# Performance work log

Hardware: AMD Instinct MI355X
Metric: run time of the kernel (lower is better)

## Reference

```python
import jax, jax.numpy as jnp
import numpy as np

H, W = 4096, 4096

# Fixed tiny kernels expressed as shifted-slice sums (exactly equivalent to
# F.conv2d with stride=1, padding=0 for these 0/1 kernels).

def _diag(x):   # [[1,0],[0,1]] -> (H-1, W-1)
    return x[:-1, :-1] + x[1:, 1:]

def _anti(x):   # [[0,1],[1,0]]
    return x[:-1, 1:] + x[1:, :-1]

def _all2(x):   # 2x2 all-ones
    return x[:-1, :-1] + x[:-1, 1:] + x[1:, :-1] + x[1:, 1:]

def _cross(x):  # 3x3 plus-shape -> (H-2, W-2)
    return x[:-2, 1:-1] + x[2:, 1:-1] + x[1:-1, :-2] + x[1:-1, 2:]

def setup_inputs() -> dict:
    key = jax.random.key(0)
    board = jax.random.randint(key, (H, W), 0, 3, dtype=jnp.int32)
    return {"board_np": board}

def reference(board_np):
    black = (board_np == 1).astype(jnp.float32)
    white = (board_np == 2).astype(jnp.float32)
    empty = (board_np == 0).astype(jnp.float32)

    black_diag, black_anti = _diag(black), _anti(black)
    white_diag, white_anti = _diag(white), _anti(white)
    empty_diag, empty_anti = _diag(empty), _anti(empty)

    bamboo_black = ((black_diag == 2) & (empty_anti == 2)) | ((black_anti == 2) & (empty_diag == 2))
    bamboo_white = ((white_diag == 2) & (empty_anti == 2)) | ((white_anti == 2) & (empty_diag == 2))

    black_s2, white_s2, empty_s2 = _all2(black), _all2(white), _all2(empty)
    # tmp_de/ae/be/ce: single-cell picks of the 2x2 window
    empty_d = empty[1:, 1:]
    empty_a = empty[:-1, :-1]
    empty_b = empty[:-1, 1:]
    empty_c = empty[1:, :-1]
    any_empty_corner = (empty_d == 1) | (empty_a == 1) | (empty_b == 1) | (empty_c == 1)

    tiger_black = (black_s2 >= 2) & any_empty_corner
    tiger_white = (white_s2 >= 2) & any_empty_corner
    empty_triangle_black = (black_s2 == 3) & (empty_s2 == 1)
    empty_triangle_white = (white_s2 == 3) & (empty_s2 == 1)

    empty_center = empty[1:-1, 1:-1]  # k_center conv
    eye_black = (empty_center == 1) & (_cross(black) == 4)
    eye_white = (empty_center == 1) & (_cross(white) == 4)

    return (bamboo_black, bamboo_white, tiger_black, tiger_white,
            empty_triangle_black, empty_triangle_white, eye_black, eye_white)
```

## Files before the change

kernel.cpp:

```cpp
#include <hip/hip_runtime.h>
#include <cstdint>


#define BW 4096
#define W1 4095
#define W2 4094
#define N1 16769025
#define N2 16760836
#define M55 0x5555u

typedef int i4a __attribute__((vector_size(16), aligned(16)));

struct Planes { unsigned pm[6]; unsigned em[2]; };

__device__ __forceinline__ Planes compute_swar(unsigned m0, unsigned m1, unsigned m2)
{
    const unsigned B0 = m0 & M55,        W0 = (m0 >> 1) & M55;
    const unsigned B1 = m1 & M55,        Wl = (m1 >> 1) & M55;
    const unsigned B2 = m2 & M55,        W2m = (m2 >> 1) & M55;
    const unsigned E0 = (B0 | W0) ^ M55;
    const unsigned E1 = (B1 | Wl) ^ M55;

    const unsigned sB0 = B0 >> 2, sB1 = B1 >> 2;
    const unsigned sW0 = W0 >> 2, sW1 = Wl >> 2;
    const unsigned sE0 = E0 >> 2, sE1 = E1 >> 2;
    const unsigned sB2 = B2 >> 2, sW2 = W2m >> 2;

    const unsigned EaEd = E0 & sE1;
    const unsigned EbEc = sE0 & E1;
    const unsigned anyE = E0 | sE0 | E1 | sE1;

    Planes r;
    {
        const unsigned P = B0 & sB0, Q = B1 & sB1;
        const unsigned Dg = B0 & sB1, Ag = sB0 & B1;
        const unsigned X = B0 & B1,  Y = sB0 & sB1;
        const unsigned ge2 = P | Q | Dg | Ag | X | Y;
        const unsigned ge3 = (P & (B1 | sB1)) | (Q & (B0 | sB0));
        r.pm[0] = (Dg & EbEc) | (Ag & EaEd);
        r.pm[2] = ge2 & anyE;
        r.pm[4] = ge3 & anyE;
        r.em[0] = sE1 & sB0 & B1 & (B1 >> 4) & sB2;
    }
    {
        const unsigned P = W0 & sW0, Q = Wl & sW1;
        const unsigned Dg = W0 & sW1, Ag = sW0 & Wl;
        const unsigned X = W0 & Wl,  Y = sW0 & sW1;
        const unsigned ge2 = P | Q | Dg | Ag | X | Y;
        const unsigned ge3 = (P & (Wl | sW1)) | (Q & (W0 | sW0));
        r.pm[1] = (Dg & EbEc) | (Ag & EaEd);
        r.pm[3] = ge2 & anyE;
        r.pm[5] = ge3 & anyE;
        r.em[1] = sE1 & sW0 & Wl & (Wl >> 4) & sW2;
    }
    return r;
}

template<int PH>
__device__ __forceinline__ void store_row(
    int* __restrict__ out, const int i, const int u, const bool has2,
    const Planes& pl)
{
    const bool fullv = (u < 1023);
    const size_t orow = (size_t)i * W1 + (u << 2);

    #pragma unroll
    for (int p = 0; p < 6; ++p) {
        const int sp = (PH - p) & 3;
        int* dst = out + (size_t)p * N1 + orow;
        if (fullv) {
            i4a s;
            s[0] = (int)((pl.pm[p] >> (2 * (sp + 0))) & 1);
            s[1] = (int)((pl.pm[p] >> (2 * (sp + 1))) & 1);
            s[2] = (int)((pl.pm[p] >> (2 * (sp + 2))) & 1);
            s[3] = (int)((pl.pm[p] >> (2 * (sp + 3))) & 1);
            *(i4a*)(dst + sp) = s;
        } else {
            #pragma unroll
            for (int k = 0; k < 3 - sp; ++k)
                dst[sp + k] = (int)((pl.pm[p] >> (2 * (sp + k))) & 1);
        }
        if (u == 0) {
            #pragma unroll
            for (int k = 0; k < sp; ++k)
                dst[k] = (int)((pl.pm[p] >> (2 * k)) & 1);
        }
    }

    if (has2) {
        const int e = (PH & 1) ? 0 : 2;
        int* d0 = out + (size_t)6 * N1 + (size_t)i * W2 + (u << 2);
        int* d1 = d0 + N2;
        if (fullv) {
            i4a s0, s1;
            #pragma unroll
            for (int k = 0; k < 4; ++k) {
                s0[k] = (int)((pl.em[0] >> (2 * (e + k))) & 1);
                s1[k] = (int)((pl.em[1] >> (2 * (e + k))) & 1);
            }
            *(i4a*)(d0 + e) = s0;
            *(i4a*)(d1 + e) = s1;
        } else if (e == 0) {
            #pragma unroll
            for (int k = 0; k < 2; ++k) {
                d0[k] = (int)((pl.em[0] >> (2 * k)) & 1);
                d1[k] = (int)((pl.em[1] >> (2 * k)) & 1);
            }
        }
        if (u == 0) {
            #pragma unroll
            for (int k = 0; k < e; ++k) {
                d0[k] = (int)((pl.em[0] >> (2 * k)) & 1);
                d1[k] = (int)((pl.em[1] >> (2 * k)) & 1);
            }
        }
    }
}

__global__ __launch_bounds__(256)
void motif_kernel(const int* __restrict__ board, int* __restrict__ out) {
    const int u  = blockIdx.x * 256 + threadIdx.x;
    const int i0 = blockIdx.y << 2;
    const int base = u << 2;
    const bool fullv = (u < 1023);
    const bool last = (i0 == W1 - 3);

    const int* pr[6];
    #pragma unroll
    for (int j = 0; j < 6; ++j) {
        int r = i0 + j; if (r > W1) r = W1;
        pr[j] = board + (size_t)r * BW + base;
    }
    i4a v[6], x[6];
    #pragma unroll
    for (int j = 0; j < 6; ++j) v[j] = *(const i4a*)pr[j];
    #pragma unroll
    for (int j = 0; j < 6; ++j) x[j] = (i4a){0,0,0,0};
    if (fullv) {
        #pragma unroll
        for (int j = 0; j < 6; ++j) x[j] = *(const i4a*)(pr[j] + 4);
    }

    auto pack = [](const i4a& vv, const i4a& xx) -> unsigned {
        return (unsigned)(vv[0] | (vv[1] << 2) | (vv[2] << 4) | (vv[3] << 6)
                        | (xx[0] << 8) | (xx[1] << 10) | (xx[2] << 12) | (xx[3] << 14));
    };
    unsigned m[6];
    #pragma unroll
    for (int j = 0; j < 6; ++j) m[j] = pack(v[j], x[j]);

    {
        Planes P = compute_swar(m[0], m[1], m[2]);
        store_row<0>(out, i0, u, true, P);
    }
    {
        Planes P = compute_swar(m[1], m[2], m[3]);
        store_row<1>(out, i0 + 1, u, true, P);
    }
    {
        Planes P = compute_swar(m[2], m[3], m[4]);
        store_row<2>(out, i0 + 2, u, !last, P);
    }
    if (!last) {
        Planes P = compute_swar(m[3], m[4], m[5]);
        store_row<3>(out, i0 + 3, u, true, P);
    }
}

extern "C" void kernel_launch(void* const* d_in, const int* in_sizes, int n_in,
                              void* d_out, int out_size, void* d_ws, size_t ws_size,
                              hipStream_t stream) {
    const int* board = (const int*)d_in[0];
    int* out = (int*)d_out;

    dim3 block(256, 1, 1);
    dim3 grid(4, 1024, 1);
    motif_kernel<<<grid, block, 0, stream>>>(board, out);
}
```

Baseline: 593.7 us.

## Split into bit-packed pack kernel and linear streaming expand kernel

Replaces the single fused kernel with two passes when a workspace is available. The first computes all eight motif planes as packed bits into a workspace of about 16 MB. The second walks the flat output linearly, decoding plane, row and column per 4-element chunk, so every store is a contiguous, aligned 16-byte write instead of the misaligned per-row stores used before. The cost is an extra launch, integer divisions per chunk and the bit-buffer round trip. The old kernel is kept as a fallback when no workspace is given.

Result: faster. 578.7 us, median of 2 (-2.5%).

```diff
diff --git a/kernel.cpp b/kernel.cpp
--- a/kernel.cpp
+++ b/kernel.cpp
@@ -5,8 +5,11 @@
 #define BW 4096
 #define W1 4095
 #define W2 4094
-#define N1 16769025
-#define N2 16760836
+#define N1 16769025u
+#define N2 16760836u
+#define TOTAL 134135822u
+#define PS 524160u
+#define NEED_BYTES 16773120u
 #define M55 0x5555u
 
 typedef int i4a __attribute__((vector_size(16), aligned(16)));
@@ -15,16 +18,16 @@
 
 __device__ __forceinline__ Planes compute_swar(unsigned m0, unsigned m1, unsigned m2)
 {
-    const unsigned B0 = m0 & M55,        W0 = (m0 >> 1) & M55;
+    const unsigned B0 = m0 & M55,        Wt = (m0 >> 1) & M55;
     const unsigned B1 = m1 & M55,        Wl = (m1 >> 1) & M55;
-    const unsigned B2 = m2 & M55,        W2m = (m2 >> 1) & M55;
-    const unsigned E0 = (B0 | W0) ^ M55;
+    const unsigned B2 = m2 & M55,        Wb = (m2 >> 1) & M55;
+    const unsigned E0 = (B0 | Wt) ^ M55;
     const unsigned E1 = (B1 | Wl) ^ M55;
 
     const unsigned sB0 = B0 >> 2, sB1 = B1 >> 2;
-    const unsigned sW0 = W0 >> 2, sW1 = Wl >> 2;
+    const unsigned sW0 = Wt >> 2, sW1 = Wl >> 2;
     const unsigned sE0 = E0 >> 2, sE1 = E1 >> 2;
-    const unsigned sB2 = B2 >> 2, sW2 = W2m >> 2;
+    const unsigned sB2 = B2 >> 2, sW2 = Wb >> 2;
 
     const unsigned EaEd = E0 & sE1;
     const unsigned EbEc = sE0 & E1;
@@ -43,11 +46,11 @@
         r.em[0] = sE1 & sB0 & B1 & (B1 >> 4) & sB2;
     }
     {
-        const unsigned P = W0 & sW0, Q = Wl & sW1;
-        const unsigned Dg = W0 & sW1, Ag = sW0 & Wl;
-        const unsigned X = W0 & Wl,  Y = sW0 & sW1;
+        const unsigned P = Wt & sW0, Q = Wl & sW1;
+        const unsigned Dg = Wt & sW1, Ag = sW0 & Wl;
+        const unsigned X = Wt & Wl,  Y = sW0 & sW1;
         const unsigned ge2 = P | Q | Dg | Ag | X | Y;
-        const unsigned ge3 = (P & (Wl | sW1)) | (Q & (W0 | sW0));
+        const unsigned ge3 = (P & (Wl | sW1)) | (Q & (Wt | sW0));
         r.pm[1] = (Dg & EbEc) | (Ag & EaEd);
         r.pm[3] = ge2 & anyE;
         r.pm[5] = ge3 & anyE;
@@ -55,6 +58,140 @@
     }
     return r;
 }
+
+
+__device__ __forceinline__ unsigned nib4(unsigned x) {
+    unsigned t = x & 0x55u;
+    t = (t | (t >> 1)) & 0x33u;
+    t = (t | (t >> 2)) & 0x0Fu;
+    return t;
+}
+
+__global__ __launch_bounds__(256)
+void pack_kernel(const int* __restrict__ board, uint32_t* __restrict__ bits)
+{
+    __shared__ uint8_t nib[32][256];
+    const int tid = threadIdx.x;
+    const int u   = blockIdx.x * 256 + tid;
+    const int i0  = blockIdx.y << 2;
+    const int base = u << 2;
+    const bool fullv = (u < 1023);
+
+    const int* pr6[6];
+    #pragma unroll
+    for (int j = 0; j < 6; ++j) {
+        int r = i0 + j; if (r > W1) r = W1;
+        pr6[j] = board + (size_t)r * BW + base;
+    }
+    i4a v[6], x[6];
+    #pragma unroll
+    for (int j = 0; j < 6; ++j) v[j] = *(const i4a*)pr6[j];
+    #pragma unroll
+    for (int j = 0; j < 6; ++j) x[j] = (i4a){0,0,0,0};
+    if (fullv) {
+        #pragma unroll
+        for (int j = 0; j < 6; ++j) x[j] = *(const i4a*)(pr6[j] + 4);
+    }
+
+    auto pack = [](const i4a& vv, const i4a& xx) -> unsigned {
+        return (unsigned)(vv[0] | (vv[1] << 2) | (vv[2] << 4) | (vv[3] << 6)
+                        | (xx[0] << 8) | (xx[1] << 10) | (xx[2] << 12) | (xx[3] << 14));
+    };
+    unsigned m[6];
+    #pragma unroll
+    for (int j = 0; j < 6; ++j) m[j] = pack(v[j], x[j]);
+
+    #pragma unroll
+    for (int r = 0; r < 4; ++r) {
+        Planes P = compute_swar(m[r], m[r + 1], m[r + 2]);
+        #pragma unroll
+        for (int p = 0; p < 6; ++p) nib[r * 8 + p][tid] = (uint8_t)nib4(P.pm[p]);
+        nib[r * 8 + 6][tid] = (uint8_t)nib4(P.em[0]);
+        nib[r * 8 + 7][tid] = (uint8_t)nib4(P.em[1]);
+    }
+    __syncthreads();
+
+    #pragma unroll
+    for (int k = 0; k < 4; ++k) {
+        const int wg  = tid + 256 * k;
+        const int pr  = wg >> 5, w_in = wg & 31;
+        const int r   = pr >> 3, p = pr & 7;
+        const int row = i0 + r;
+        const bool valid = (p < 6) ? (row <= 4094) : (row <= 4093);
+        if (valid) {
+            uint64_t t = *(const uint64_t*)&nib[pr][w_in * 8];
+            t &= 0x0F0F0F0F0F0F0F0Full;
+            t = (t | (t >> 4))  & 0x00FF00FF00FF00FFull;
+            t = (t | (t >> 8))  & 0x0000FFFF0000FFFFull;
+            t = (t | (t >> 16));
+            bits[(size_t)p * PS + (size_t)row * 128u
+                 + (unsigned)(blockIdx.x * 32 + w_in)] = (uint32_t)t;
+        }
+    }
+}
+
+__device__ __forceinline__ void decode(uint32_t e, uint32_t& p, uint32_t& row,
+                                       uint32_t& col, uint32_t& width)
+{
+    if (e < 6u * N1) {
+        p = e / N1;
+        const uint32_t rem = e - p * N1;
+        row = rem / W1;
+        col = rem - row * W1;
+        width = W1;
+    } else {
+        const uint32_t q  = e - 6u * N1;
+        const uint32_t pp = q / N2;
+        const uint32_t rem = q - pp * N2;
+        p = 6u + pp;
+        row = rem / W2;
+        col = rem - row * W2;
+        width = W2;
+    }
+}
+
+__global__ __launch_bounds__(256)
+void expand_kernel(const uint32_t* __restrict__ bits, int* __restrict__ out)
+{
+    const uint32_t c = blockIdx.x * 256u + threadIdx.x;
+    const uint32_t o = c * 4u;
+    if (o >= TOTAL) return;
+
+    uint32_t p, row, col, width;
+    decode(o, p, row, col, width);
+
+    if (col + 3u < width && o + 4u <= TOTAL) {
+        const uint32_t* wrow = bits + p * PS + row * 128u;
+        const uint32_t lo = col >> 5, sh = col & 31u;
+        const uint32_t w0 = wrow[lo];
+        const uint32_t w1 = wrow[lo + 1];
+        const uint32_t bv = (uint32_t)(((uint64_t)w0 | ((uint64_t)w1 << 32)) >> sh);
+        i4a s;
+        s[0] = (int)(bv & 1u);
+        s[1] = (int)((bv >> 1) & 1u);
+        s[2] = (int)((bv >> 2) & 1u);
+        s[3] = (int)((bv >> 3) & 1u);
+        *(i4a*)(out + o) = s;
+    } else {
+        int vals[4];
+        #pragma unroll
+        for (int k = 0; k < 4; ++k) {
+            const uint32_t e = o + (uint32_t)k;
+            if (e < TOTAL) {
+                uint32_t pp, rr, cc, ww;
+                decode(e, pp, rr, cc, ww);
+                vals[k] = (int)((bits[pp * PS + rr * 128u + (cc >> 5)] >> (cc & 31u)) & 1u);
+            } else vals[k] = 0;
+        }
+        if (o + 4u <= TOTAL) {
+            i4a s; s[0] = vals[0]; s[1] = vals[1]; s[2] = vals[2]; s[3] = vals[3];
+            *(i4a*)(out + o) = s;
+        } else {
+            for (uint32_t k = 0; o + k < TOTAL; ++k) out[o + k] = vals[k];
+        }
+    }
+}
+
 
 template<int PH>
 __device__ __forceinline__ void store_row(
@@ -149,23 +286,17 @@
     #pragma unroll
     for (int j = 0; j < 6; ++j) m[j] = pack(v[j], x[j]);
 
-    {
-        Planes P = compute_swar(m[0], m[1], m[2]);
-        store_row<0>(out, i0, u, true, P);
-    }
-    {
-        Planes P = compute_swar(m[1], m[2], m[3]);
-        store_row<1>(out, i0 + 1, u, true, P);
-    }
-    {
-        Planes P = compute_swar(m[2], m[3], m[4]);
-        store_row<2>(out, i0 + 2, u, !last, P);
-    }
+    {   Planes P = compute_swar(m[0], m[1], m[2]);
+        store_row<0>(out, i0, u, true, P); }
+    {   Planes P = compute_swar(m[1], m[2], m[3]);
+        store_row<1>(out, i0 + 1, u, true, P); }
+    {   Planes P = compute_swar(m[2], m[3], m[4]);
+        store_row<2>(out, i0 + 2, u, !last, P); }
     if (!last) {
         Planes P = compute_swar(m[3], m[4], m[5]);
-        store_row<3>(out, i0 + 3, u, true, P);
-    }
-}
+        store_row<3>(out, i0 + 3, u, true, P); }
+}
+
 
 extern "C" void kernel_launch(void* const* d_in, const int* in_sizes, int n_in,
                               void* d_out, int out_size, void* d_ws, size_t ws_size,
@@ -173,7 +304,13 @@
     const int* board = (const int*)d_in[0];
     int* out = (int*)d_out;
 
-    dim3 block(256, 1, 1);
-    dim3 grid(4, 1024, 1);
-    motif_kernel<<<grid, block, 0, stream>>>(board, out);
-}
+    if (d_ws != nullptr && ws_size >= (size_t)NEED_BYTES) {
+        uint32_t* bits = (uint32_t*)d_ws;
+        pack_kernel<<<dim3(4, 1024, 1), dim3(256, 1, 1), 0, stream>>>(board, bits);
+        const uint32_t chunks = (TOTAL + 3u) / 4u;
+        const uint32_t eblocks = (chunks + 255u) / 256u;
+        expand_kernel<<<dim3(eblocks, 1, 1), dim3(256, 1, 1), 0, stream>>>(bits, out);
+    } else {
+        motif_kernel<<<dim3(4, 1024, 1), dim3(256, 1, 1), 0, stream>>>(board, out);
+    }
+}
```

## Switch to output-indexed kernel with one aligned 4-wide store per thread

Applied to the files above, without the earlier changes.

Replaces the row-tiled kernel, in which each thread loaded six board rows and wrote all eight planes with misaligned partial stores, with a flat kernel where each thread owns four consecutive output elements. Each thread decodes plane, row and column by integer division, then loads only the few board cells it needs and runs the SWAR logic for a single plane before doing one aligned 16-byte store. This removes the unaligned and scalar edge writes. In exchange every plane reloads the board, giving about eight times more input reads (mostly cache hits), plus per-thread divisions and a scalar fallback for chunks that straddle rows.

Result: slower. 661.4 us (+11.4%).

```diff
diff --git a/kernel.cpp b/kernel.cpp
--- a/kernel.cpp
+++ b/kernel.cpp
@@ -5,8 +5,9 @@
 #define BW 4096
 #define W1 4095
 #define W2 4094
-#define N1 16769025
-#define N2 16760836
+#define N1 16769025u
+#define N2 16760836u
+#define TOTAL 134135822u
 #define M55 0x5555u
 
 typedef int i4a __attribute__((vector_size(16), aligned(16)));
@@ -15,16 +16,16 @@
 
 __device__ __forceinline__ Planes compute_swar(unsigned m0, unsigned m1, unsigned m2)
 {
-    const unsigned B0 = m0 & M55,        W0 = (m0 >> 1) & M55;
+    const unsigned B0 = m0 & M55,        Wt = (m0 >> 1) & M55;
     const unsigned B1 = m1 & M55,        Wl = (m1 >> 1) & M55;
-    const unsigned B2 = m2 & M55,        W2m = (m2 >> 1) & M55;
-    const unsigned E0 = (B0 | W0) ^ M55;
+    const unsigned B2 = m2 & M55,        Wb = (m2 >> 1) & M55;
+    const unsigned E0 = (B0 | Wt) ^ M55;
     const unsigned E1 = (B1 | Wl) ^ M55;
 
     const unsigned sB0 = B0 >> 2, sB1 = B1 >> 2;
-    const unsigned sW0 = W0 >> 2, sW1 = Wl >> 2;
+    const unsigned sW0 = Wt >> 2, sW1 = Wl >> 2;
     const unsigned sE0 = E0 >> 2, sE1 = E1 >> 2;
-    const unsigned sB2 = B2 >> 2, sW2 = W2m >> 2;
+    const unsigned sB2 = B2 >> 2, sW2 = Wb >> 2;
 
     const unsigned EaEd = E0 & sE1;
     const unsigned EbEc = sE0 & E1;
@@ -43,11 +44,11 @@
         r.em[0] = sE1 & sB0 & B1 & (B1 >> 4) & sB2;
     }
     {
-        const unsigned P = W0 & sW0, Q = Wl & sW1;
-        const unsigned Dg = W0 & sW1, Ag = sW0 & Wl;
-        const unsigned X = W0 & Wl,  Y = sW0 & sW1;
+        const unsigned P = Wt & sW0, Q = Wl & sW1;
+        const unsigned Dg = Wt & sW1, Ag = sW0 & Wl;
+        const unsigned X = Wt & Wl,  Y = sW0 & sW1;
         const unsigned ge2 = P | Q | Dg | Ag | X | Y;
-        const unsigned ge3 = (P & (Wl | sW1)) | (Q & (W0 | sW0));
+        const unsigned ge3 = (P & (Wl | sW1)) | (Q & (Wt | sW0));
         r.pm[1] = (Dg & EbEc) | (Ag & EaEd);
         r.pm[3] = ge2 & anyE;
         r.pm[5] = ge3 & anyE;
@@ -56,114 +57,112 @@
     return r;
 }
 
-template<int PH>
-__device__ __forceinline__ void store_row(
-    int* __restrict__ out, const int i, const int u, const bool has2,
-    const Planes& pl)
+__device__ __forceinline__ void decode(uint32_t e, uint32_t& p, uint32_t& row,
+                                       uint32_t& col, uint32_t& width)
 {
-    const bool fullv = (u < 1023);
-    const size_t orow = (size_t)i * W1 + (u << 2);
-
-    #pragma unroll
-    for (int p = 0; p < 6; ++p) {
-        const int sp = (PH - p) & 3;
-        int* dst = out + (size_t)p * N1 + orow;
-        if (fullv) {
-            i4a s;
-            s[0] = (int)((pl.pm[p] >> (2 * (sp + 0))) & 1);
-            s[1] = (int)((pl.pm[p] >> (2 * (sp + 1))) & 1);
-            s[2] = (int)((pl.pm[p] >> (2 * (sp + 2))) & 1);
-            s[3] = (int)((pl.pm[p] >> (2 * (sp + 3))) & 1);
-            *(i4a*)(dst + sp) = s;
-        } else {
-            #pragma unroll
-            for (int k = 0; k < 3 - sp; ++k)
-                dst[sp + k] = (int)((pl.pm[p] >> (2 * (sp + k))) & 1);
-        }
-        if (u == 0) {
-            #pragma unroll
-            for (int k = 0; k < sp; ++k)
-                dst[k] = (int)((pl.pm[p] >> (2 * k)) & 1);
-        }
-    }
-
-    if (has2) {
-        const int e = (PH & 1) ? 0 : 2;
-        int* d0 = out + (size_t)6 * N1 + (size_t)i * W2 + (u << 2);
-        int* d1 = d0 + N2;
-        if (fullv) {
-            i4a s0, s1;
-            #pragma unroll
-            for (int k = 0; k < 4; ++k) {
-                s0[k] = (int)((pl.em[0] >> (2 * (e + k))) & 1);
-                s1[k] = (int)((pl.em[1] >> (2 * (e + k))) & 1);
-            }
-            *(i4a*)(d0 + e) = s0;
-            *(i4a*)(d1 + e) = s1;
-        } else if (e == 0) {
-            #pragma unroll
-            for (int k = 0; k < 2; ++k) {
-                d0[k] = (int)((pl.em[0] >> (2 * k)) & 1);
-                d1[k] = (int)((pl.em[1] >> (2 * k)) & 1);
-            }
-        }
-        if (u == 0) {
-            #pragma unroll
-            for (int k = 0; k < e; ++k) {
-                d0[k] = (int)((pl.em[0] >> (2 * k)) & 1);
-                d1[k] = (int)((pl.em[1] >> (2 * k)) & 1);
-            }
-        }
+    if (e < 6u * N1) {
+        p = e / N1;
+        const uint32_t rem = e - p * N1;
+        row = rem / W1;
+        col = rem - row * W1;
+        width = W1;
+    } else {
+        const uint32_t q  = e - 6u * N1;
+        const uint32_t pp = q / N2;
+        const uint32_t rem = q - pp * N2;
+        p = 6u + pp;
+        row = rem / W2;
+        col = rem - row * W2;
+        width = W2;
     }
 }
 
+__device__ __forceinline__ int one_out(const int* __restrict__ board,
+                                       uint32_t p, uint32_t row, uint32_t col)
+{
+    if (p < 6u) {
+        const int a = board[(size_t)row * BW + col];
+        const int b = board[(size_t)row * BW + col + 1];
+        const int c = board[(size_t)(row + 1) * BW + col];
+        const int d = board[(size_t)(row + 1) * BW + col + 1];
+        const int nb = (a == 1) + (b == 1) + (c == 1) + (d == 1);
+        const int nw = (a == 2) + (b == 2) + (c == 2) + (d == 2);
+        const int ne = 4 - nb - nw;
+        switch (p) {
+        case 0: return ((a==1 && d==1 && b==0 && c==0) || (b==1 && c==1 && a==0 && d==0));
+        case 1: return ((a==2 && d==2 && b==0 && c==0) || (b==2 && c==2 && a==0 && d==0));
+        case 2: return (nb >= 2 && ne >= 1);
+        case 3: return (nw >= 2 && ne >= 1);
+        case 4: return (nb == 3 && ne == 1);
+        default: return (nw == 3 && ne == 1);
+        }
+    }
+    const int st = (p == 6u) ? 1 : 2;
+    const size_t r1 = (size_t)(row + 1) * BW;
+    return (board[r1 + col + 1] == 0
+         && board[(size_t)row * BW + col + 1] == st
+         && board[(size_t)(row + 2) * BW + col + 1] == st
+         && board[r1 + col] == st
+         && board[r1 + col + 2] == st);
+}
+
 __global__ __launch_bounds__(256)
-void motif_kernel(const int* __restrict__ board, int* __restrict__ out) {
-    const int u  = blockIdx.x * 256 + threadIdx.x;
-    const int i0 = blockIdx.y << 2;
-    const int base = u << 2;
-    const bool fullv = (u < 1023);
-    const bool last = (i0 == W1 - 3);
+void direct_kernel(const int* __restrict__ board, int* __restrict__ out)
+{
+    const uint32_t c = blockIdx.x * 256u + threadIdx.x;
+    const uint32_t o = c * 4u;
+    if (o >= TOTAL) return;
 
-    const int* pr[6];
-    #pragma unroll
-    for (int j = 0; j < 6; ++j) {
-        int r = i0 + j; if (r > W1) r = W1;
-        pr[j] = board + (size_t)r * BW + base;
-    }
-    i4a v[6], x[6];
-    #pragma unroll
-    for (int j = 0; j < 6; ++j) v[j] = *(const i4a*)pr[j];
-    #pragma unroll
-    for (int j = 0; j < 6; ++j) x[j] = (i4a){0,0,0,0};
-    if (fullv) {
+    uint32_t p, row, col, width;
+    decode(o, p, row, col, width);
+
+    if (col + 3u < width && o + 4u <= TOTAL) {
+        const int* r0p = board + (size_t)row * BW + col;
+        const int* r1p = r0p + BW;
+        unsigned m0 = 0, m1 = 0, m2 = 0;
         #pragma unroll
-        for (int j = 0; j < 6; ++j) x[j] = *(const i4a*)(pr[j] + 4);
-    }
-
-    auto pack = [](const i4a& vv, const i4a& xx) -> unsigned {
-        return (unsigned)(vv[0] | (vv[1] << 2) | (vv[2] << 4) | (vv[3] << 6)
-                        | (xx[0] << 8) | (xx[1] << 10) | (xx[2] << 12) | (xx[3] << 14));
-    };
-    unsigned m[6];
-    #pragma unroll
-    for (int j = 0; j < 6; ++j) m[j] = pack(v[j], x[j]);
-
-    {
-        Planes P = compute_swar(m[0], m[1], m[2]);
-        store_row<0>(out, i0, u, true, P);
-    }
-    {
-        Planes P = compute_swar(m[1], m[2], m[3]);
-        store_row<1>(out, i0 + 1, u, true, P);
-    }
-    {
-        Planes P = compute_swar(m[2], m[3], m[4]);
-        store_row<2>(out, i0 + 2, u, !last, P);
-    }
-    if (!last) {
-        Planes P = compute_swar(m[3], m[4], m[5]);
-        store_row<3>(out, i0 + 3, u, true, P);
+        for (int k = 0; k < 5; ++k) {
+            m0 |= ((unsigned)r0p[k]) << (2 * k);
+            m1 |= ((unsigned)r1p[k]) << (2 * k);
+        }
+        if (p >= 6u) {
+            const int* r2p = r1p + BW;
+            m1 |= ((unsigned)r1p[5]) << 10;
+            #pragma unroll
+            for (int k = 0; k < 5; ++k)
+                m2 |= ((unsigned)r2p[k]) << (2 * k);
+        }
+        const Planes P = compute_swar(m0, m1, m2);
+        unsigned w;
+        switch (p) {
+        case 0: w = P.pm[0]; break;  case 1: w = P.pm[1]; break;
+        case 2: w = P.pm[2]; break;  case 3: w = P.pm[3]; break;
+        case 4: w = P.pm[4]; break;  case 5: w = P.pm[5]; break;
+        case 6: w = P.em[0]; break;  default: w = P.em[1]; break;
+        }
+        i4a s;
+        s[0] = (int)(w & 1u);
+        s[1] = (int)((w >> 2) & 1u);
+        s[2] = (int)((w >> 4) & 1u);
+        s[3] = (int)((w >> 6) & 1u);
+        *(i4a*)(out + o) = s;
+    } else {
+        int vals[4];
+        #pragma unroll
+        for (int k = 0; k < 4; ++k) {
+            const uint32_t e = o + (uint32_t)k;
+            if (e < TOTAL) {
+                uint32_t pp, rr, cc, ww;
+                decode(e, pp, rr, cc, ww);
+                vals[k] = one_out(board, pp, rr, cc);
+            } else vals[k] = 0;
+        }
+        if (o + 4u <= TOTAL) {
+            i4a s; s[0] = vals[0]; s[1] = vals[1]; s[2] = vals[2]; s[3] = vals[3];
+            *(i4a*)(out + o) = s;
+        } else {
+            for (uint32_t k = 0; o + k < TOTAL; ++k) out[o + k] = vals[k];
+        }
     }
 }
 
@@ -173,7 +172,7 @@
     const int* board = (const int*)d_in[0];
     int* out = (int*)d_out;
 
-    dim3 block(256, 1, 1);
-    dim3 grid(4, 1024, 1);
-    motif_kernel<<<grid, block, 0, stream>>>(board, out);
+    const uint32_t chunks  = (TOTAL + 3u) / 4u;
+    const uint32_t nblocks = (chunks + 255u) / 256u;
+    direct_kernel<<<dim3(nblocks, 1, 1), dim3(256, 1, 1), 0, stream>>>(board, out);
 }
```
